# Kernel tuning notes

Measured on AMD Instinct MI355X. Metric: run time of the kernel, lower is better.

## Reference

```python
import jax, jax.numpy as jnp
import numpy as np

VOCAB, D_MODEL, MAX_LEN = 32000, 1024, 4096
B, S = 4, 2048


def make_pe(max_len, d_model):
    pos = np.arange(max_len)[:, None].astype(np.float32)
    div = np.exp(np.arange(0, d_model, 2).astype(np.float32) * -(np.log(10000.0) / d_model))
    pe = np.zeros((max_len, d_model), dtype=np.float32)
    pe[:, 0::2] = np.sin(pos * div)
    pe[:, 1::2] = np.cos(pos * div)
    return jnp.asarray(pe)


def setup_inputs() -> dict:
    key = jax.random.key(0)
    k1, k2, k3 = jax.random.split(key, 3)
    text = jax.random.randint(k1, (B, S), 0, VOCAB)
    W = jax.random.normal(k2, (D_MODEL, VOCAB), dtype=jnp.float32) * 0.02
    b = jax.random.normal(k3, (D_MODEL,), dtype=jnp.float32) * 0.02
    pe = make_pe(MAX_LEN, D_MODEL)
    return {"text": text, "W": W, "b": b, "pe": pe}


def reference(text, W, b, pe):
    # one_hot(text) @ W.T + b  ==  gather of W columns: out[b,s,:] = W[:, text[b,s]] + b
    emb = jnp.take(W.T, text, axis=0)          # [B, S, d_model]
    out = emb + b + pe[: text.shape[-1]]       # positional add, broadcast over batch
    return out  # dropout is identity in eval mode
```

## Files before the change

kernel.cpp:

```cpp
#include <hip/hip_runtime.h>


#define VOCAB  32000
#define DMODEL 1024
#define S_LEN  2048
#define B_N    4
#define NTOK   (B_N * S_LEN)
#define VT     64
#define DT     64
#define NBIN   (VOCAB / VT)
#define NDT    (DMODEL / DT)
#define NBLK   (NBIN * NDT)
#define LSTRIDE (VT + 1)

__global__ __launch_bounds__(1024) void bin_k(const int* __restrict__ text,
                                              int2* __restrict__ sorted,
                                              int* __restrict__ tile_off) {
    __shared__ int cnt[512];
    __shared__ int scn[512];
    const int t = threadIdx.x;
    if (t < 512) cnt[t] = 0;
    __syncthreads();

    int toks[8];
    #pragma unroll
    for (int j = 0; j < 8; ++j) {
        toks[j] = text[t * 8 + j];
        atomicAdd(&cnt[toks[j] >> 6], 1);
    }
    __syncthreads();

    if (t < 512) scn[t] = cnt[t];
    __syncthreads();
    for (int off = 1; off < 512; off <<= 1) {
        int x = 0;
        if (t < 512 && t >= off) x = scn[t - off];
        __syncthreads();
        if (t < 512) scn[t] += x;
        __syncthreads();
    }
    if (t < 512) {
        const int start = scn[t] - cnt[t];
        tile_off[t] = start;
        cnt[t] = start;
    }
    __syncthreads();

    #pragma unroll
    for (int j = 0; j < 8; ++j) {
        const int tok = toks[j];
        const int slot = atomicAdd(&cnt[tok >> 6], 1);
        sorted[slot] = make_int2(tok, t * 8 + j);
    }
}

__global__ __launch_bounds__(256, 8) void gather_k(const int2* __restrict__ sorted,
                                                   const int* __restrict__ tile_off,
                                                   const float* __restrict__ W,
                                                   const float* __restrict__ bias,
                                                   const float* __restrict__ pe,
                                                   float* __restrict__ out) {
    __shared__ float lds[DT * LSTRIDE];

    const int bid = blockIdx.x;
    const int vt = bid >> 4;
    const int dt = bid & (NDT - 1);
    const int v0 = vt * VT;
    const int d0 = dt * DT;
    const int t  = threadIdx.x;

    {
        const int c4 = t & 15;
        const int r0 = t >> 4;
        #pragma unroll
        for (int i = 0; i < 4; ++i) {
            const int row = r0 + i * 16;
            const float4 w4 = *reinterpret_cast<const float4*>(
                W + (size_t)(d0 + row) * VOCAB + v0 + c4 * 4);
            float* lp = lds + row * LSTRIDE + c4 * 4;
            lp[0] = w4.x; lp[1] = w4.y; lp[2] = w4.z; lp[3] = w4.w;
        }
    }
    __syncthreads();

    const int a0 = tile_off[vt];
    const int a1 = tile_off[vt + 1];
    const int lane = t & 63;
    const int wv   = t >> 6;
    const float bv = bias[d0 + lane];

    for (int i = a0 + wv; i < a1; i += 4) {
        const int2 p = sorted[i];
        const int tokl = p.x - v0;
        const int bs   = p.y;
        const int s    = bs & (S_LEN - 1);
        const float wval = lds[lane * LSTRIDE + tokl];
        const float pv = pe[(size_t)s * DMODEL + d0 + lane];
        out[(size_t)bs * DMODEL + d0 + lane] = wval + bv + pv;
    }
}

__global__ __launch_bounds__(256) void embed_pe_direct(const int* __restrict__ text,
                                                       const float* __restrict__ W,
                                                       const float* __restrict__ bias,
                                                       const float* __restrict__ pe,
                                                       float* __restrict__ out) {
    const int bs = blockIdx.x;
    const int s  = bs & (S_LEN - 1);
    const int tok = text[bs];
    const int d = threadIdx.x << 2;
    const float4 b4 = *reinterpret_cast<const float4*>(bias + d);
    const float4 p4 = *reinterpret_cast<const float4*>(pe + (size_t)s * DMODEL + d);
    const float* wcol = W + (size_t)d * VOCAB + tok;
    float4 o;
    o.x = wcol[0]                 + b4.x + p4.x;
    o.y = wcol[(size_t)VOCAB]     + b4.y + p4.y;
    o.z = wcol[(size_t)2 * VOCAB] + b4.z + p4.z;
    o.w = wcol[(size_t)3 * VOCAB] + b4.w + p4.w;
    *reinterpret_cast<float4*>(out + (size_t)bs * DMODEL + d) = o;
}

extern "C" void kernel_launch(void* const* d_in, const int* in_sizes, int n_in,
                              void* d_out, int out_size, void* d_ws, size_t ws_size,
                              hipStream_t stream) {
    const int*   text = (const int*)d_in[0];
    const float* W    = (const float*)d_in[1];
    const float* bias = (const float*)d_in[2];
    const float* pe   = (const float*)d_in[3];
    float*       out  = (float*)d_out;

    const size_t sorted_bytes = (size_t)NTOK * sizeof(int2);
    const size_t off_bytes    = 513 * sizeof(int);
    if (ws_size < sorted_bytes + off_bytes) {
        embed_pe_direct<<<NTOK, 256, 0, stream>>>(text, W, bias, pe, out);
        return;
    }

    int2* sorted   = (int2*)d_ws;
    int*  tile_off = (int*)((char*)d_ws + sorted_bytes);

    bin_k   <<<1, 1024, 0, stream>>>(text, sorted, tile_off);
    gather_k<<<NBLK, 256, 0, stream>>>(sorted, tile_off, W, bias, pe, out);
}
```

Measured before the change: 40.17 us.

## Split binning into parallel histogram, scan and scatter kernels; add nontemporal hints

Replaces the single-block token binning kernel with a memset, a grid-wide global-atomic histogram, a one-block scan and a grid-wide global-atomic scatter, so the sort no longer runs on one CU. The gather kernel now uses nontemporal loads for the streamed W tile and nontemporal stores for the output, to reduce cache pollution on the main bandwidth-bound pass. The price is more launches, a memset, and global atomic contention on 500 bins, which could outweigh the serial cost being removed.

```diff
diff --git a/kernel.cpp b/kernel.cpp
--- a/kernel.cpp
+++ b/kernel.cpp
@@ -13,44 +13,43 @@
 #define NBLK   (NBIN * NDT)
 #define LSTRIDE (VT + 1)
 
-__global__ __launch_bounds__(1024) void bin_k(const int* __restrict__ text,
-                                              int2* __restrict__ sorted,
+typedef float f4 __attribute__((ext_vector_type(4)));
+
+__global__ __launch_bounds__(256) void hist_k(const int* __restrict__ text,
+                                              int* __restrict__ hist) {
+    const int i = blockIdx.x * 256 + threadIdx.x;
+    if (i < NTOK) atomicAdd(&hist[text[i] >> 6], 1);
+}
+
+__global__ __launch_bounds__(512) void scan_k(int* __restrict__ hist,
                                               int* __restrict__ tile_off) {
-    __shared__ int cnt[512];
     __shared__ int scn[512];
     const int t = threadIdx.x;
-    if (t < 512) cnt[t] = 0;
-    __syncthreads();
-
-    int toks[8];
-    #pragma unroll
-    for (int j = 0; j < 8; ++j) {
-        toks[j] = text[t * 8 + j];
-        atomicAdd(&cnt[toks[j] >> 6], 1);
-    }
-    __syncthreads();
-
-    if (t < 512) scn[t] = cnt[t];
+    const int cnt = (t < NBIN) ? hist[t] : 0;
+    scn[t] = cnt;
     __syncthreads();
     for (int off = 1; off < 512; off <<= 1) {
-        int x = 0;
-        if (t < 512 && t >= off) x = scn[t - off];
+        int x = (t >= off) ? scn[t - off] : 0;
         __syncthreads();
-        if (t < 512) scn[t] += x;
+        scn[t] += x;
         __syncthreads();
     }
-    if (t < 512) {
-        const int start = scn[t] - cnt[t];
+    if (t < NBIN) {
+        const int start = scn[t] - cnt;
         tile_off[t] = start;
-        cnt[t] = start;
+        hist[t] = start;
     }
-    __syncthreads();
+    if (t == 0) tile_off[NBIN] = NTOK;
+}
 
-    #pragma unroll
-    for (int j = 0; j < 8; ++j) {
-        const int tok = toks[j];
-        const int slot = atomicAdd(&cnt[tok >> 6], 1);
-        sorted[slot] = make_int2(tok, t * 8 + j);
+__global__ __launch_bounds__(256) void scatter_k(const int* __restrict__ text,
+                                                 int* __restrict__ cursor,
+                                                 int2* __restrict__ sorted) {
+    const int i = blockIdx.x * 256 + threadIdx.x;
+    if (i < NTOK) {
+        const int tok = text[i];
+        const int slot = atomicAdd(&cursor[tok >> 6], 1);
+        sorted[slot] = make_int2(tok, i);
     }
 }
 
@@ -75,8 +74,9 @@
         #pragma unroll
         for (int i = 0; i < 4; ++i) {
             const int row = r0 + i * 16;
-            const float4 w4 = *reinterpret_cast<const float4*>(
-                W + (size_t)(d0 + row) * VOCAB + v0 + c4 * 4);
+            const f4 w4 = __builtin_nontemporal_load(
+                reinterpret_cast<const f4*>(
+                    W + (size_t)(d0 + row) * VOCAB + v0 + c4 * 4));
             float* lp = lds + row * LSTRIDE + c4 * 4;
             lp[0] = w4.x; lp[1] = w4.y; lp[2] = w4.z; lp[3] = w4.w;
         }
@@ -96,7 +96,8 @@
         const int s    = bs & (S_LEN - 1);
         const float wval = lds[lane * LSTRIDE + tokl];
         const float pv = pe[(size_t)s * DMODEL + d0 + lane];
-        out[(size_t)bs * DMODEL + d0 + lane] = wval + bv + pv;
+        __builtin_nontemporal_store(wval + bv + pv,
+                                    out + (size_t)bs * DMODEL + d0 + lane);
     }
 }
 
@@ -130,15 +131,20 @@
     float*       out  = (float*)d_out;
 
     const size_t sorted_bytes = (size_t)NTOK * sizeof(int2);
-    const size_t off_bytes    = 513 * sizeof(int);
-    if (ws_size < sorted_bytes + off_bytes) {
+    const size_t off_bytes    = (NBIN + 1) * sizeof(int);
+    const size_t hist_bytes   = NBIN * sizeof(int);
+    if (ws_size < sorted_bytes + off_bytes + hist_bytes) {
         embed_pe_direct<<<NTOK, 256, 0, stream>>>(text, W, bias, pe, out);
         return;
     }
 
     int2* sorted   = (int2*)d_ws;
     int*  tile_off = (int*)((char*)d_ws + sorted_bytes);
+    int*  hist     = (int*)((char*)d_ws + sorted_bytes + off_bytes);
 
-    bin_k   <<<1, 1024, 0, stream>>>(text, sorted, tile_off);
-    gather_k<<<NBLK, 256, 0, stream>>>(sorted, tile_off, W, bias, pe, out);
+    (void)hipMemsetAsync(hist, 0, hist_bytes, stream);
+    hist_k   <<<NTOK / 256, 256, 0, stream>>>(text, hist);
+    scan_k   <<<1, 512, 0, stream>>>(hist, tile_off);
+    scatter_k<<<NTOK / 256, 256, 0, stream>>>(text, hist, sorted);
+    gather_k <<<NBLK, 256, 0, stream>>>(sorted, tile_off, W, bias, pe, out);
 }
```

After: 55.72 us. 1.39x slower.

## Transpose LDS W tile for float4 gathers and use wavefront-shuffle bin scan

Applied to the files above, without the earlier changes.

The gather kernel now stores the W tile transposed in LDS (token-major, padded rows). Each token is handled by 16 lanes doing float4 LDS reads, float4 pe loads and float4 output stores, so one wave covers 4 tokens instead of one 64-lane scalar pass per token. This cuts instruction count and the number of memory transactions per token. The single-block binning kernel replaces its 512-wide shared-memory Hillis-Steele scan, which needed many block-wide barriers, with a per-thread 8-element local scan plus a 64-lane shuffle scan. The transposed LDS fill may introduce some bank conflicts on writes.

```diff
diff --git a/kernel.cpp b/kernel.cpp
--- a/kernel.cpp
+++ b/kernel.cpp
@@ -11,13 +11,13 @@
 #define NBIN   (VOCAB / VT)
 #define NDT    (DMODEL / DT)
 #define NBLK   (NBIN * NDT)
-#define LSTRIDE (VT + 1)
+#define LROW   (DT + 4)
 
 __global__ __launch_bounds__(1024) void bin_k(const int* __restrict__ text,
                                               int2* __restrict__ sorted,
                                               int* __restrict__ tile_off) {
     __shared__ int cnt[512];
-    __shared__ int scn[512];
+    __shared__ int cur[512];
     const int t = threadIdx.x;
     if (t < 512) cnt[t] = 0;
     __syncthreads();
@@ -30,26 +30,32 @@
     }
     __syncthreads();
 
-    if (t < 512) scn[t] = cnt[t];
-    __syncthreads();
-    for (int off = 1; off < 512; off <<= 1) {
-        int x = 0;
-        if (t < 512 && t >= off) x = scn[t - off];
-        __syncthreads();
-        if (t < 512) scn[t] += x;
-        __syncthreads();
-    }
-    if (t < 512) {
-        const int start = scn[t] - cnt[t];
-        tile_off[t] = start;
-        cnt[t] = start;
+    if (t < 64) {
+        const int base = t * 8;
+        int loc[8];
+        int s = 0;
+        #pragma unroll
+        for (int j = 0; j < 8; ++j) { loc[j] = s; s += cnt[base + j]; }
+        const int own = s;
+        #pragma unroll
+        for (int off = 1; off < 64; off <<= 1) {
+            const int n = __shfl_up(s, off, 64);
+            if (t >= off) s += n;
+        }
+        const int excl = s - own;
+        #pragma unroll
+        for (int j = 0; j < 8; ++j) {
+            const int v = excl + loc[j];
+            cur[base + j] = v;
+            if (base + j <= NBIN) tile_off[base + j] = v;
+        }
     }
     __syncthreads();
 
     #pragma unroll
     for (int j = 0; j < 8; ++j) {
         const int tok = toks[j];
-        const int slot = atomicAdd(&cnt[tok >> 6], 1);
+        const int slot = atomicAdd(&cur[tok >> 6], 1);
         sorted[slot] = make_int2(tok, t * 8 + j);
     }
 }
@@ -60,7 +66,7 @@
                                                    const float* __restrict__ bias,
                                                    const float* __restrict__ pe,
                                                    float* __restrict__ out) {
-    __shared__ float lds[DT * LSTRIDE];
+    __shared__ float lds[VT][LROW];
 
     const int bid = blockIdx.x;
     const int vt = bid >> 4;
@@ -77,8 +83,10 @@
             const int row = r0 + i * 16;
             const float4 w4 = *reinterpret_cast<const float4*>(
                 W + (size_t)(d0 + row) * VOCAB + v0 + c4 * 4);
-            float* lp = lds + row * LSTRIDE + c4 * 4;
-            lp[0] = w4.x; lp[1] = w4.y; lp[2] = w4.z; lp[3] = w4.w;
+            lds[c4 * 4 + 0][row] = w4.x;
+            lds[c4 * 4 + 1][row] = w4.y;
+            lds[c4 * 4 + 2][row] = w4.z;
+            lds[c4 * 4 + 3][row] = w4.w;
         }
     }
     __syncthreads();
@@ -87,16 +95,24 @@
     const int a1 = tile_off[vt + 1];
     const int lane = t & 63;
     const int wv   = t >> 6;
-    const float bv = bias[d0 + lane];
+    const int grp  = lane >> 4;
+    const int ld   = lane & 15;
+    const int d    = d0 + ld * 4;
+    const float4 b4 = *reinterpret_cast<const float4*>(bias + d);
 
-    for (int i = a0 + wv; i < a1; i += 4) {
+    for (int i = a0 + wv * 4 + grp; i < a1; i += 16) {
         const int2 p = sorted[i];
         const int tokl = p.x - v0;
         const int bs   = p.y;
         const int s    = bs & (S_LEN - 1);
-        const float wval = lds[lane * LSTRIDE + tokl];
-        const float pv = pe[(size_t)s * DMODEL + d0 + lane];
-        out[(size_t)bs * DMODEL + d0 + lane] = wval + bv + pv;
+        const float4 w4 = *reinterpret_cast<const float4*>(&lds[tokl][ld * 4]);
+        const float4 p4 = *reinterpret_cast<const float4*>(pe + (size_t)s * DMODEL + d);
+        float4 o;
+        o.x = w4.x + b4.x + p4.x;
+        o.y = w4.y + b4.y + p4.y;
+        o.z = w4.z + b4.z + p4.z;
+        o.w = w4.w + b4.w + p4.w;
+        *reinterpret_cast<float4*>(out + (size_t)bs * DMODEL + d) = o;
     }
 }
 
@@ -130,7 +146,7 @@
     float*       out  = (float*)d_out;
 
     const size_t sorted_bytes = (size_t)NTOK * sizeof(int2);
-    const size_t off_bytes    = 513 * sizeof(int);
+    const size_t off_bytes    = (NBIN + 1) * sizeof(int);
     if (ws_size < sorted_bytes + off_bytes) {
         embed_pe_direct<<<NTOK, 256, 0, stream>>>(text, W, bias, pe, out);
         return;
```

New measurement: 39.01 us, median of 2. 1.03x faster.
